# Kernel tuning notes

Hardware: AMD Instinct MI355X
Metric: run time of the kernel (lower is better)

The kernel has to match this reference:

```python
import jax, jax.numpy as jnp
import numpy as np

D = 4096      # feature_dim
L = 24        # num_vision_layers
N = 576       # patches per layer (24x24 grid)
T = 128       # text tokens
RED = D // 4  # DSU reduced dim
TOPK = 128
FINAL_K = 64
THRESH = 2.0
EPS = 1e-6


def _ln(x, eps=1e-5):
    mu = jnp.mean(x, axis=-1, keepdims=True)
    var = jnp.mean((x - mu) ** 2, axis=-1, keepdims=True)
    return (x - mu) / jnp.sqrt(var + eps)


def setup_inputs() -> dict:
    key = jax.random.key(0)
    ks = jax.random.split(key, 8)
    w = lambda k, shape: jax.random.normal(k, shape, jnp.float32) * 0.02
    z = lambda shape: jnp.zeros(shape, jnp.float32)
    return {
        "text_features": jax.random.normal(ks[0], (T, D), jnp.float32),
        "proj": jax.random.normal(ks[1], (L, N, D), jnp.float32),
        "Wq": w(ks[2], (D, D)),
        "Wk": w(ks[3], (D, D)),
        "ln_w": jnp.ones((D,), jnp.float32),
        "ln_b": z((D,)),
        "W1_w": w(ks[4], (RED, 3 * D)), "W1_b": z((RED,)),
        "Wc_w": w(ks[5], (D, RED)), "Wc_b": z((D,)),
        "Wi_w": w(ks[6], (D, RED)), "Wi_b": z((D,)),
        "Wf_w": w(ks[7], (D, RED)), "Wf_b": z((D,)),
        "bc": z((D,)), "bi": z((D,)), "bf": z((D,)),
    }


def _scores_z(text_features, proj, Wq, Wk, ln_w, ln_b,
              W1_w, W1_b, Wc_w, Wc_b, Wi_w, Wi_b, Wf_w, Wf_b, bc, bi, bf):
    # DSU recurrence over layers on (D,) vectors
    text_global = _ln(jnp.mean(text_features, axis=0))  # [D]
    y = jnp.mean(proj, axis=1)                           # [L, D]

    def step(c_prev, y_l):
        combined = jnp.concatenate([jax.nn.sigmoid(c_prev), y_l, text_global])
        s = jax.nn.relu(combined @ W1_w.T + W1_b)
        c_t = jnp.tanh(s @ Wc_w.T + Wc_b + bc)
        i = jax.nn.sigmoid(s @ Wi_w.T + Wi_b + bi)
        f = jax.nn.sigmoid(s @ Wf_w.T + Wf_b + bf)
        c = f * c_prev + i * c_t
        return c, c

    _, contexts = jax.lax.scan(step, jnp.zeros((D,), proj.dtype), y)
    c_final = contexts[-2]
    q = _ln(c_final @ Wq.T) * ln_w + ln_b              # [D]
    k = _ln(jnp.einsum('lnd,ed->lne', proj, Wk)) * ln_w + ln_b  # [L,N,D]
    scores = jnp.einsum('lne,e->ln', k, q)             # [L, N]
    mu = jnp.mean(scores, axis=-1, keepdims=True)
    sd = jnp.std(scores, axis=-1, keepdims=True)       # unbiased=False
    return (scores - mu) / (sd + EPS)


def _select(scores_z_np):
    """Host-side, data-dependent top-k budget allocation (mirrors torch code).
    Returns flat (layer_id, patch_idx) arrays of the final selected evidence."""
    Lc, Nc = scores_z_np.shape
    focus = (-2) % Lc
    conf = scores_z_np.max(axis=-1)
    active = [li for li in range(Lc) if li == focus or conf[li] > THRESH]
    focus_cand = min(TOPK // 2, Nc)
    k_per = [0] * Lc
    k_per[focus] = focus_cand
    rest = max(TOPK - focus_cand, 0)
    other = [li for li in active if li != focus]
    if other and rest > 0:
        cv = conf[other]
        w = np.exp(cv - cv.max()); w = w / w.sum()
        alloc = np.floor(w * rest).astype(np.int64)
        rem = rest - int(alloc.sum())
        for j in np.argsort(-w):
            if rem <= 0:
                break
            alloc[j] += 1; rem -= 1
        for j, li in enumerate(other):
            if alloc[j] > 0:
                k_per[li] = min(int(alloc[j]), Nc)
    li_flat, idx_flat, sc_flat = [], [], []
    for li in range(Lc):
        k_li = min(k_per[li], Nc)
        if k_li <= 0:
            continue
        idx = np.argsort(-scores_z_np[li])[:k_li]   # topk, sorted desc
        li_flat.append(np.full(k_li, li, np.int64))
        idx_flat.append(idx)
        sc_flat.append(scores_z_np[li][idx])
    li_flat = np.concatenate(li_flat)
    idx_flat = np.concatenate(idx_flat)
    sc = np.concatenate(sc_flat)
    M = sc.shape[0]
    final_k = min(FINAL_K, M)
    focus_min = min(FINAL_K // 2, final_k)
    fidx = np.nonzero(li_flat == focus)[0]
    selected = []
    if fidx.size > 0 and focus_min > 0:
        order = np.argsort(-sc[fidx])[:min(focus_min, fidx.size)]
        selected.append(fidx[order])
    remain = final_k - (selected[0].size if selected else 0)
    if remain > 0:
        keep = np.ones(M, bool)
        if selected:
            keep[selected[0]] = False
        cand = np.nonzero(keep)[0]
        order = np.argsort(-sc[cand])[:min(remain, cand.size)]
        selected.append(cand[order])
    sel = np.concatenate(selected) if selected else np.zeros(0, np.int64)
    sel = sel[np.argsort(-sc[sel])]  # final re-sort by score desc
    return li_flat[sel], idx_flat[sel]


def reference(text_features, proj, Wq, Wk, ln_w, ln_b,
              W1_w, W1_b, Wc_w, Wc_b, Wi_w, Wi_b, Wf_w, Wf_b, bc, bi, bf):
    scores_z = _scores_z(text_features, proj, Wq, Wk, ln_w, ln_b,
                         W1_w, W1_b, Wc_w, Wc_b, Wi_w, Wi_b, Wf_w, Wf_b,
                         bc, bi, bf)
    li, idx = _select(np.asarray(scores_z))
    # evidence tokens: gather selected patches across layers -> [final_k, D]
    return proj[jnp.asarray(li), jnp.asarray(idx)]
```

## Files before the change

kernel.cpp:

```cpp
#include <hip/hip_runtime.h>
#include <stdint.h>
#include <math.h>

#define DD 4096
#define LL 24
#define NP 576
#define TT 128
#define RED 1024
#define MTOT (LL * NP)

#define NEG_INF (-3.402823466e+38f)

typedef __bf16 bf16x8 __attribute__((ext_vector_type(8)));
typedef float f32x4 __attribute__((ext_vector_type(4)));

__device__ inline unsigned short bf16_rn(float a) {
  unsigned u = __float_as_uint(a);
  return (unsigned short)((u + 0x7FFFu + ((u >> 16) & 1u)) >> 16);
}
__device__ inline void bsplit(float a, unsigned short& h, unsigned short& l) {
  unsigned short hb = bf16_rn(a);
  float hf = __uint_as_float(((unsigned)hb) << 16);
  h = hb;
  l = bf16_rn(a - hf);
}
__device__ inline float wave_sum(float v) {
  #pragma unroll
  for (int off = 32; off > 0; off >>= 1) v += __shfl_down(v, off);
  return v;
}
__device__ inline float sigm(float x) { return 1.0f / (1.0f + expf(-x)); }

__device__ inline float np_sum(const float* a, int n) {
  if (n < 8) {
    float r = 0.0f;
    for (int i = 0; i < n; ++i) r += a[i];
    return r;
  }
  float r0 = a[0], r1 = a[1], r2 = a[2], r3 = a[3];
  float r4 = a[4], r5 = a[5], r6 = a[6], r7 = a[7];
  int i = 8;
  for (; i + 8 <= n; i += 8) {
    r0 += a[i + 0]; r1 += a[i + 1]; r2 += a[i + 2]; r3 += a[i + 3];
    r4 += a[i + 4]; r5 += a[i + 5]; r6 += a[i + 6]; r7 += a[i + 7];
  }
  float res = ((r0 + r1) + (r2 + r3)) + ((r4 + r5) + (r6 + r7));
  for (; i < n; ++i) res += a[i];
  return res;
}

__global__ __launch_bounds__(256) void k_text_mean(const float4* __restrict__ tf, float4* __restrict__ tmean) {
  int i = blockIdx.x * 256 + threadIdx.x;
  float a = 0, b = 0, c = 0, d = 0;
  for (int t = 0; t < TT; ++t) {
    float4 v = tf[(size_t)t * (DD / 4) + i];
    a += v.x; b += v.y; c += v.z; d += v.w;
  }
  float4 o; o.x = a * (1.0f / TT); o.y = b * (1.0f / TT); o.z = c * (1.0f / TT); o.w = d * (1.0f / TT);
  tmean[i] = o;
}

__global__ __launch_bounds__(256) void k_ln_vec(const float* __restrict__ in, float* __restrict__ out) {
  __shared__ float red[256];
  int tid = threadIdx.x;
  float s = 0;
  for (int i = tid; i < DD; i += 256) s += in[i];
  red[tid] = s; __syncthreads();
  for (int o = 128; o > 0; o >>= 1) { if (tid < o) red[tid] += red[tid + o]; __syncthreads(); }
  float mu = red[0] / (float)DD;
  __syncthreads();
  float v = 0;
  for (int i = tid; i < DD; i += 256) { float d0 = in[i] - mu; v += d0 * d0; }
  red[tid] = v; __syncthreads();
  for (int o = 128; o > 0; o >>= 1) { if (tid < o) red[tid] += red[tid + o]; __syncthreads(); }
  float isd = 1.0f / sqrtf(red[0] / (float)DD + 1e-5f);
  for (int i = tid; i < DD; i += 256) out[i] = (in[i] - mu) * isd;
}

__global__ __launch_bounds__(256) void k_y_mean(const float4* __restrict__ proj, float4* __restrict__ y) {
  int i4 = blockIdx.x * 256 + threadIdx.x;
  int l = i4 >> 10;
  int d4 = i4 & 1023;
  const float4* base = proj + (size_t)l * NP * (DD / 4) + d4;
  float a = 0, b = 0, c = 0, d = 0;
  for (int n = 0; n < NP; ++n) {
    float4 v = base[(size_t)n * (DD / 4)];
    a += v.x; b += v.y; c += v.z; d += v.w;
  }
  float4 o; o.x = a * (1.0f / NP); o.y = b * (1.0f / NP); o.z = c * (1.0f / NP); o.w = d * (1.0f / NP);
  y[i4] = o;
}

__global__ __launch_bounds__(256) void k_base1(const float* __restrict__ W1, const float* __restrict__ W1bias,
                                               const float* __restrict__ y, const float* __restrict__ tg,
                                               float* __restrict__ base1) {
  const int r = blockIdx.x;
  const int tid = threadIdx.x;
  const float* rowB = W1 + (size_t)r * (3 * DD) + DD;
  const float* rowC = W1 + (size_t)r * (3 * DD) + 2 * DD;
  float part[LL];
  #pragma unroll
  for (int l = 0; l < LL; ++l) part[l] = 0.0f;
  float ptg = 0.0f;
  for (int d = tid; d < DD; d += 256) {
    float wb = rowB[d], wc = rowC[d];
    ptg += wc * tg[d];
    #pragma unroll
    for (int l = 0; l < LL; ++l) part[l] += wb * y[l * DD + d];
  }
  __shared__ float red[4 * 25];
  int wv = tid >> 6, lane = tid & 63;
  #pragma unroll
  for (int l = 0; l < LL; ++l) {
    float v = wave_sum(part[l]);
    if (lane == 0) red[wv * 25 + l] = v;
  }
  {
    float v = wave_sum(ptg);
    if (lane == 0) red[wv * 25 + 24] = v;
  }
  __syncthreads();
  if (tid < LL) {
    float v = red[tid] + red[25 + tid] + red[50 + tid] + red[75 + tid];
    float t = red[24] + red[49] + red[74] + red[99];
    base1[tid * RED + r] = v + t + W1bias[r];
  }
}

__global__ __launch_bounds__(256) void k_init(float* __restrict__ c0, float* __restrict__ sg0) {
  int i = blockIdx.x * 256 + threadIdx.x;
  if (i < DD) { c0[i] = 0.0f; sg0[i] = 0.5f; }
}

__global__ __launch_bounds__(256) void k_dsu_A(const float4* __restrict__ W1, const float4* __restrict__ sigc,
                                               const float* __restrict__ base1l, float* __restrict__ s_out) {
  const int r = blockIdx.x;
  const int tid = threadIdx.x;
  const float4* row = W1 + (size_t)r * (3 * DD / 4);
  float acc = 0.0f;
  #pragma unroll
  for (int i = tid; i < DD / 4; i += 256) {
    float4 w = row[i], x = sigc[i];
    acc += w.x * x.x + w.y * x.y + w.z * x.z + w.w * x.w;
  }
  acc = wave_sum(acc);
  __shared__ float red[4];
  if ((tid & 63) == 0) red[tid >> 6] = acc;
  __syncthreads();
  if (tid == 0) {
    float v = red[0] + red[1] + red[2] + red[3] + base1l[r];
    s_out[r] = fmaxf(v, 0.0f);
  }
}

__global__ __launch_bounds__(192) void k_dsu_B(const float4* __restrict__ Wc, const float4* __restrict__ Wi,
                                               const float4* __restrict__ Wf, const float* __restrict__ Wcb,
                                               const float* __restrict__ Wib, const float* __restrict__ Wfb,
                                               const float* __restrict__ bcv, const float* __restrict__ biv,
                                               const float* __restrict__ bfv, const float4* __restrict__ s,
                                               const float* __restrict__ c_in, float* __restrict__ c_out,
                                               float* __restrict__ sigc_out) {
  const int d = blockIdx.x;
  const int wv = threadIdx.x / 64, lane = threadIdx.x & 63;
  const float4* W = (wv == 0) ? Wc : (wv == 1) ? Wi : Wf;
  const float4* row = W + (size_t)d * (RED / 4);
  float acc = 0.0f;
  #pragma unroll
  for (int i = lane; i < RED / 4; i += 64) {
    float4 w = row[i], x = s[i];
    acc += w.x * x.x + w.y * x.y + w.z * x.z + w.w * x.w;
  }
  acc = wave_sum(acc);
  __shared__ float us[3];
  if (lane == 0) us[wv] = acc;
  __syncthreads();
  if (threadIdx.x == 0) {
    float ct = tanhf(us[0] + Wcb[d] + bcv[d]);
    float ig = sigm(us[1] + Wib[d] + biv[d]);
    float fg = sigm(us[2] + Wfb[d] + bfv[d]);
    float c = fg * c_in[d] + ig * ct;
    c_out[d] = c;
    sigc_out[d] = sigm(c);
  }
}

__global__ __launch_bounds__(256) void k_qvec(const float4* __restrict__ Wq, const float4* __restrict__ c,
                                              float* __restrict__ u) {
  const int e = blockIdx.x;
  const int tid = threadIdx.x;
  const float4* row = Wq + (size_t)e * (DD / 4);
  float acc = 0.0f;
  #pragma unroll
  for (int i = tid; i < DD / 4; i += 256) {
    float4 w = row[i], x = c[i];
    acc += w.x * x.x + w.y * x.y + w.z * x.z + w.w * x.w;
  }
  acc = wave_sum(acc);
  __shared__ float red[4];
  if ((tid & 63) == 0) red[tid >> 6] = acc;
  __syncthreads();
  if (tid == 0) u[e] = red[0] + red[1] + red[2] + red[3];
}

__global__ __launch_bounds__(256) void k_qln(const float* __restrict__ u, const float* __restrict__ lnw,
                                             const float* __restrict__ lnb, float* __restrict__ wtil,
                                             float* __restrict__ scal) {
  __shared__ float red[256];
  int tid = threadIdx.x;
  float s = 0;
  for (int i = tid; i < DD; i += 256) s += u[i];
  red[tid] = s; __syncthreads();
  for (int o = 128; o > 0; o >>= 1) { if (tid < o) red[tid] += red[tid + o]; __syncthreads(); }
  float mu = red[0] / (float)DD;
  __syncthreads();
  float v = 0;
  for (int i = tid; i < DD; i += 256) { float d0 = u[i] - mu; v += d0 * d0; }
  red[tid] = v; __syncthreads();
  for (int o = 128; o > 0; o >>= 1) { if (tid < o) red[tid] += red[tid + o]; __syncthreads(); }
  float isd = 1.0f / sqrtf(red[0] / (float)DD + 1e-5f);
  __syncthreads();
  float a = 0, b = 0;
  for (int i = tid; i < DD; i += 256) {
    float q = (u[i] - mu) * isd * lnw[i] + lnb[i];
    float wt = lnw[i] * q;
    wtil[i] = wt;
    a += wt;
    b += lnb[i] * q;
  }
  red[tid] = a; __syncthreads();
  for (int o = 128; o > 0; o >>= 1) { if (tid < o) red[tid] += red[tid + o]; __syncthreads(); }
  float alpha = red[0];
  __syncthreads();
  red[tid] = b; __syncthreads();
  for (int o = 128; o > 0; o >>= 1) { if (tid < o) red[tid] += red[tid + o]; __syncthreads(); }
  if (tid == 0) { scal[0] = alpha; scal[1] = red[0]; }
}

__global__ __launch_bounds__(256) void k_split(const float4* __restrict__ src, ushort4* __restrict__ hi,
                                               ushort4* __restrict__ lo) {
  size_t i = (size_t)blockIdx.x * 256 + threadIdx.x;
  float4 v = src[i];
  ushort4 h, l;
  bsplit(v.x, h.x, l.x);
  bsplit(v.y, h.y, l.y);
  bsplit(v.z, h.z, l.z);
  bsplit(v.w, h.w, l.w);
  hi[i] = h;
  lo[i] = l;
}

#define GLDS16(g, l)                                                                     \
  __builtin_amdgcn_global_load_lds((__attribute__((address_space(1))) void*)(void*)(g),  \
                                   (__attribute__((address_space(3))) void*)(l), 16, 0, 0)

__global__ __launch_bounds__(256) void k_gemm(const unsigned short* __restrict__ Ahi,
                                              const unsigned short* __restrict__ Alo,
                                              const unsigned short* __restrict__ Bhi,
                                              const unsigned short* __restrict__ Blo,
                                              const float* __restrict__ wtilde,
                                              float* __restrict__ partials) {
  __shared__ __align__(16) unsigned short sAh[4096];
  __shared__ __align__(16) unsigned short sAl[4096];
  __shared__ __align__(16) unsigned short sBh[4096];
  __shared__ __align__(16) unsigned short sBl[4096];

  const int tid = threadIdx.x;
  const int w = tid >> 6, lane = tid & 63;
  const int n0 = blockIdx.x * 128, m0 = blockIdx.y * 128;

  const int flat = w * 1024 + lane * 16;
  const int row0 = flat >> 6;
  const int colb = (flat & 63) >> 1;

  const unsigned short* gA0h = Ahi + (size_t)(m0 + row0) * DD + colb;
  const unsigned short* gA1h = gA0h + (size_t)64 * DD;
  const unsigned short* gA0l = Alo + (size_t)(m0 + row0) * DD + colb;
  const unsigned short* gA1l = gA0l + (size_t)64 * DD;
  const unsigned short* gB0h = Bhi + (size_t)(n0 + row0) * DD + colb;
  const unsigned short* gB1h = gB0h + (size_t)64 * DD;
  const unsigned short* gB0l = Blo + (size_t)(n0 + row0) * DD + colb;
  const unsigned short* gB1l = gB0l + (size_t)64 * DD;

  const int r16 = lane & 15, qd = lane >> 4;
  const int wm = (w & 1) << 6, wn = (w >> 1) << 6;

  f32x4 acc[4][4];
  #pragma unroll
  for (int mi = 0; mi < 4; ++mi)
    #pragma unroll
    for (int ni = 0; ni < 4; ++ni) acc[mi][ni] = (f32x4){0.f, 0.f, 0.f, 0.f};

  for (int kk = 0; kk < DD / 32; ++kk) {
    __syncthreads();
    GLDS16(gA0h, sAh + w * 512);
    GLDS16(gA1h, sAh + 2048 + w * 512);
    GLDS16(gA0l, sAl + w * 512);
    GLDS16(gA1l, sAl + 2048 + w * 512);
    GLDS16(gB0h, sBh + w * 512);
    GLDS16(gB1h, sBh + 2048 + w * 512);
    GLDS16(gB0l, sBl + w * 512);
    GLDS16(gB1l, sBl + 2048 + w * 512);
    gA0h += 32; gA1h += 32; gA0l += 32; gA1l += 32;
    gB0h += 32; gB1h += 32; gB0l += 32; gB1l += 32;
    __syncthreads();

    bf16x8 ah[4], al[4], bh[4], bl[4];
    #pragma unroll
    for (int mi = 0; mi < 4; ++mi) {
      int off = (wm + mi * 16 + r16) * 32 + qd * 8;
      ah[mi] = *(const bf16x8*)(sAh + off);
      al[mi] = *(const bf16x8*)(sAl + off);
    }
    #pragma unroll
    for (int ni = 0; ni < 4; ++ni) {
      int off = (wn + ni * 16 + r16) * 32 + qd * 8;
      bh[ni] = *(const bf16x8*)(sBh + off);
      bl[ni] = *(const bf16x8*)(sBl + off);
    }
    #pragma unroll
    for (int mi = 0; mi < 4; ++mi)
      #pragma unroll
      for (int ni = 0; ni < 4; ++ni)
        acc[mi][ni] = __builtin_amdgcn_mfma_f32_16x16x32_bf16(ah[mi], bh[ni], acc[mi][ni], 0, 0, 0);
    #pragma unroll
    for (int mi = 0; mi < 4; ++mi)
      #pragma unroll
      for (int ni = 0; ni < 4; ++ni)
        acc[mi][ni] = __builtin_amdgcn_mfma_f32_16x16x32_bf16(ah[mi], bl[ni], acc[mi][ni], 0, 0, 0);
    #pragma unroll
    for (int mi = 0; mi < 4; ++mi)
      #pragma unroll
      for (int ni = 0; ni < 4; ++ni)
        acc[mi][ni] = __builtin_amdgcn_mfma_f32_16x16x32_bf16(al[mi], bh[ni], acc[mi][ni], 0, 0, 0);
  }

  float wt[4];
  #pragma unroll
  for (int ni = 0; ni < 4; ++ni) wt[ni] = wtilde[n0 + wn + ni * 16 + r16];

  __syncthreads();
  float* epi = (float*)sAh;
  #pragma unroll
  for (int mi = 0; mi < 4; ++mi) {
    #pragma unroll
    for (int j = 0; j < 4; ++j) {
      float sv = 0, sv2 = 0, svw = 0;
      #pragma unroll
      for (int ni = 0; ni < 4; ++ni) {
        float v = acc[mi][ni][j];
        sv += v;
        sv2 += v * v;
        svw += v * wt[ni];
      }
      #pragma unroll
      for (int off = 1; off < 16; off <<= 1) {
        sv += __shfl_xor(sv, off);
        sv2 += __shfl_xor(sv2, off);
        svw += __shfl_xor(svw, off);
      }
      if (r16 == 0) {
        int row = wm + mi * 16 + qd * 4 + j;
        int half = w >> 1;
        epi[(half * 128 + row) * 3 + 0] = sv;
        epi[(half * 128 + row) * 3 + 1] = sv2;
        epi[(half * 128 + row) * 3 + 2] = svw;
      }
    }
  }
  __syncthreads();
  if (tid < 128) {
    size_t base = (size_t)(m0 + tid) * 96 + (size_t)blockIdx.x * 3;
    #pragma unroll
    for (int c = 0; c < 3; ++c) partials[base + c] = epi[tid * 3 + c] + epi[(128 + tid) * 3 + c];
  }
}

__global__ __launch_bounds__(256) void k_scorefin(const float* __restrict__ partials,
                                                  const float* __restrict__ scal,
                                                  float* __restrict__ scores) {
  int m = blockIdx.x * 256 + threadIdx.x;
  const float* p = partials + (size_t)m * 96;
  float s1 = 0, s2 = 0, sw = 0;
  #pragma unroll
  for (int j = 0; j < 32; ++j) {
    s1 += p[j * 3 + 0];
    s2 += p[j * 3 + 1];
    sw += p[j * 3 + 2];
  }
  float mu = s1 * (1.0f / DD);
  float var = s2 * (1.0f / DD) - mu * mu;
  float isd = 1.0f / sqrtf(var + 1e-5f);
  scores[m] = isd * (sw - mu * scal[0]) + scal[1];
}

__global__ __launch_bounds__(256) void k_zscore(const float* __restrict__ scores, float* __restrict__ z,
                                                float* __restrict__ conf) {
  const int l = blockIdx.x;
  const int tid = threadIdx.x;
  const float* s = scores + l * NP;
  __shared__ float red[256];
  float a = 0;
  for (int i = tid; i < NP; i += 256) a += s[i];
  red[tid] = a; __syncthreads();
  for (int o = 128; o > 0; o >>= 1) { if (tid < o) red[tid] += red[tid + o]; __syncthreads(); }
  float mu = red[0] / (float)NP;
  __syncthreads();
  float v = 0;
  for (int i = tid; i < NP; i += 256) { float d0 = s[i] - mu; v += d0 * d0; }
  red[tid] = v; __syncthreads();
  for (int o = 128; o > 0; o >>= 1) { if (tid < o) red[tid] += red[tid + o]; __syncthreads(); }
  float sd = sqrtf(red[0] / (float)NP);
  float inv = 1.0f / (sd + 1e-6f);
  __syncthreads();
  float mx = NEG_INF;
  for (int i = tid; i < NP; i += 256) {
    float zz = (s[i] - mu) * inv;
    z[l * NP + i] = zz;
    mx = fmaxf(mx, zz);
  }
  red[tid] = mx; __syncthreads();
  for (int o = 128; o > 0; o >>= 1) { if (tid < o) red[tid] = fmaxf(red[tid], red[tid + o]); __syncthreads(); }
  if (tid == 0) conf[l] = red[0];
}

__global__ __launch_bounds__(64) void k_select(const float* __restrict__ z, const float* __restrict__ conf,
                                               int* __restrict__ sel_li, int* __restrict__ sel_idx) {
  const int lane = threadIdx.x;
  __shared__ int kper[24];
  __shared__ int offs[25];
  __shared__ float zb[576];
  __shared__ float csc[160];
  __shared__ int cli[160];
  __shared__ int cidx[160];
  __shared__ int taken[160];
  __shared__ int selpos[64];

  if (lane == 0) {
    const int focus = 22;
    float cf[24];
    for (int l = 0; l < 24; ++l) cf[l] = conf[l];
    int other[24]; int no = 0;
    for (int l = 0; l < 24; ++l)
      if (l != focus && cf[l] > 2.0f) other[no++] = l;
    int kp[24];
    for (int l = 0; l < 24; ++l) kp[l] = 0;
    kp[focus] = 64;
    const int rest = 64;
    if (no > 0) {
      float wv[24];
      float cmax = cf[other[0]];
      for (int j = 1; j < no; ++j) cmax = fmaxf(cmax, cf[other[j]]);
      for (int j = 0; j < no; ++j) wv[j] = (float)exp((double)(cf[other[j]] - cmax));
      float wsum = np_sum(wv, no);
      for (int j = 0; j < no; ++j) wv[j] = wv[j] / wsum;
      int alloc[24]; int asum = 0;
      for (int j = 0; j < no; ++j) { alloc[j] = (int)floorf(wv[j] * 64.0f); asum += alloc[j]; }
      int rem = rest - asum;
      int used[24];
      for (int j = 0; j < no; ++j) used[j] = 0;
      for (int t = 0; t < no && rem > 0; ++t) {
        int bj = -1; float bw = -1e38f;
        for (int j = 0; j < no; ++j)
          if (!used[j] && wv[j] > bw) { bw = wv[j]; bj = j; }
        used[bj] = 1; alloc[bj] += 1; rem -= 1;
      }
      for (int j = 0; j < no; ++j)
        if (alloc[j] > 0) kp[other[j]] = (alloc[j] < NP) ? alloc[j] : NP;
    }
    int o = 0;
    for (int l = 0; l < 24; ++l) { kper[l] = kp[l]; offs[l] = o; o += kp[l]; }
    offs[24] = o;
  }
  __syncthreads();

  for (int l = 0; l < 24; ++l) {
    const int kl = kper[l];
    if (kl == 0) continue;
    for (int i = lane; i < NP; i += 64) zb[i] = z[l * NP + i];
    __syncthreads();
    const int base = offs[l];
    for (int t = 0; t < kl; ++t) {
      float bv = NEG_INF; int bi_ = 0x7fffffff;
      for (int i = lane; i < NP; i += 64) {
        float v = zb[i];
        if (v > bv) { bv = v; bi_ = i; }
      }
      #pragma unroll
      for (int off = 32; off > 0; off >>= 1) {
        float ov = __shfl_down(bv, off);
        int oi = __shfl_down(bi_, off);
        if (ov > bv || (ov == bv && oi < bi_)) { bv = ov; bi_ = oi; }
      }
      bv = __shfl(bv, 0);
      bi_ = __shfl(bi_, 0);
      if (lane == 0) {
        csc[base + t] = bv; cli[base + t] = l; cidx[base + t] = bi_;
        zb[bi_] = NEG_INF;
      }
      __syncthreads();
    }
    __syncthreads();
  }

  const int M = offs[24];
  const int foff = offs[22];
  for (int i = lane; i < M; i += 64) taken[i] = 0;
  __syncthreads();
  if (lane < 32) { selpos[lane] = foff + lane; taken[foff + lane] = 1; }
  __syncthreads();
  for (int t = 0; t < 32; ++t) {
    float bv = NEG_INF; int bp = 0x7fffffff;
    for (int i = lane; i < M; i += 64) {
      if (!taken[i]) {
        float v = csc[i];
        if (v > bv || (v == bv && i < bp)) { bv = v; bp = i; }
      }
    }
    #pragma unroll
    for (int off = 32; off > 0; off >>= 1) {
      float ov = __shfl_down(bv, off);
      int op = __shfl_down(bp, off);
      if (ov > bv || (ov == bv && op < bp)) { bv = ov; bp = op; }
    }
    bp = __shfl(bp, 0);
    if (lane == 0) { selpos[32 + t] = bp; taken[bp] = 1; }
    __syncthreads();
  }
  if (lane == 0) {
    int a = 0, b = 32;
    for (int k = 0; k < 64; ++k) {
      bool takeA;
      if (a >= 32) takeA = false;
      else if (b >= 64) takeA = true;
      else takeA = (csc[selpos[a]] >= csc[selpos[b]]);
      int p = takeA ? selpos[a++] : selpos[b++];
      sel_li[k] = cli[p];
      sel_idx[k] = cidx[p];
    }
  }
}

__global__ __launch_bounds__(256) void k_gather(const float4* __restrict__ proj, const int* __restrict__ sel_li,
                                                const int* __restrict__ sel_idx, float4* __restrict__ out) {
  int r = blockIdx.x;
  int li = sel_li[r], idx = sel_idx[r];
  const float4* src = proj + (size_t)(li * NP + idx) * (DD / 4);
  float4* dst = out + (size_t)r * (DD / 4);
  for (int i = threadIdx.x; i < DD / 4; i += 256) dst[i] = src[i];
}

constexpr size_t OFF_AHI = 0;
constexpr size_t OFF_ALO = OFF_AHI + 113246208ull;
constexpr size_t OFF_BHI = OFF_ALO + 113246208ull;
constexpr size_t OFF_BLO = OFF_BHI + 33554432ull;
constexpr size_t OFF_PART = OFF_BLO + 33554432ull;
constexpr size_t OFF_SCORE = OFF_PART + 5308416ull;
constexpr size_t OFF_Z = OFF_SCORE + 55296ull;
constexpr size_t OFF_TMEAN = OFF_Z + 55296ull;
constexpr size_t OFF_TG = OFF_TMEAN + 16384ull;
constexpr size_t OFF_Y = OFF_TG + 16384ull;
constexpr size_t OFF_BASE1 = OFF_Y + 393216ull;
constexpr size_t OFF_CA = OFF_BASE1 + 98304ull;
constexpr size_t OFF_CB = OFF_CA + 16384ull;
constexpr size_t OFF_SGA = OFF_CB + 16384ull;
constexpr size_t OFF_SGB = OFF_SGA + 16384ull;
constexpr size_t OFF_S = OFF_SGB + 16384ull;
constexpr size_t OFF_U = OFF_S + 4096ull;
constexpr size_t OFF_WT = OFF_U + 16384ull;
constexpr size_t OFF_SCAL = OFF_WT + 16384ull;
constexpr size_t OFF_CONF = OFF_SCAL + 256ull;
constexpr size_t OFF_SELLI = OFF_CONF + 256ull;
constexpr size_t OFF_SELIX = OFF_SELLI + 256ull;

extern "C" void kernel_launch(void* const* d_in, const int* in_sizes, int n_in,
                              void* d_out, int out_size, void* d_ws, size_t ws_size,
                              hipStream_t stream) {
  (void)in_sizes; (void)n_in; (void)out_size; (void)ws_size;
  const float* tf = (const float*)d_in[0];
  const float* proj = (const float*)d_in[1];
  const float* Wq = (const float*)d_in[2];
  const float* Wk = (const float*)d_in[3];
  const float* ln_w = (const float*)d_in[4];
  const float* ln_b = (const float*)d_in[5];
  const float* W1w = (const float*)d_in[6];
  const float* W1b = (const float*)d_in[7];
  const float* Wcw = (const float*)d_in[8];
  const float* Wcb = (const float*)d_in[9];
  const float* Wiw = (const float*)d_in[10];
  const float* Wib = (const float*)d_in[11];
  const float* Wfw = (const float*)d_in[12];
  const float* Wfb = (const float*)d_in[13];
  const float* bc = (const float*)d_in[14];
  const float* bi = (const float*)d_in[15];
  const float* bf = (const float*)d_in[16];

  char* ws = (char*)d_ws;
  unsigned short* Ahi = (unsigned short*)(ws + OFF_AHI);
  unsigned short* Alo = (unsigned short*)(ws + OFF_ALO);
  unsigned short* Bhi = (unsigned short*)(ws + OFF_BHI);
  unsigned short* Blo = (unsigned short*)(ws + OFF_BLO);
  float* partials = (float*)(ws + OFF_PART);
  float* scores = (float*)(ws + OFF_SCORE);
  float* zbuf = (float*)(ws + OFF_Z);
  float* tmean = (float*)(ws + OFF_TMEAN);
  float* tg = (float*)(ws + OFF_TG);
  float* ybuf = (float*)(ws + OFF_Y);
  float* base1 = (float*)(ws + OFF_BASE1);
  float* cA = (float*)(ws + OFF_CA);
  float* cB = (float*)(ws + OFF_CB);
  float* sgA = (float*)(ws + OFF_SGA);
  float* sgB = (float*)(ws + OFF_SGB);
  float* svec = (float*)(ws + OFF_S);
  float* uvec = (float*)(ws + OFF_U);
  float* wtil = (float*)(ws + OFF_WT);
  float* scal = (float*)(ws + OFF_SCAL);
  float* conf = (float*)(ws + OFF_CONF);
  int* sel_li = (int*)(ws + OFF_SELLI);
  int* sel_idx = (int*)(ws + OFF_SELIX);

  k_text_mean<<<4, 256, 0, stream>>>((const float4*)tf, (float4*)tmean);
  k_ln_vec<<<1, 256, 0, stream>>>(tmean, tg);
  k_y_mean<<<96, 256, 0, stream>>>((const float4*)proj, (float4*)ybuf);
  k_base1<<<1024, 256, 0, stream>>>(W1w, W1b, ybuf, tg, base1);
  k_init<<<16, 256, 0, stream>>>(cA, sgA);

  float* cbuf[2] = {cA, cB};
  float* sgbuf[2] = {sgA, sgB};
  for (int l = 0; l < 23; ++l) {
    int pi = l & 1;
    k_dsu_A<<<1024, 256, 0, stream>>>((const float4*)W1w, (const float4*)sgbuf[pi],
                                      base1 + (size_t)l * RED, svec);
    k_dsu_B<<<4096, 192, 0, stream>>>((const float4*)Wcw, (const float4*)Wiw, (const float4*)Wfw,
                                      Wcb, Wib, Wfb, bc, bi, bf,
                                      (const float4*)svec, cbuf[pi], cbuf[1 - pi], sgbuf[1 - pi]);
  }
  k_qvec<<<4096, 256, 0, stream>>>((const float4*)Wq, (const float4*)cbuf[1], uvec);
  k_qln<<<1, 256, 0, stream>>>(uvec, ln_w, ln_b, wtil, scal);

  k_split<<<55296, 256, 0, stream>>>((const float4*)proj, (ushort4*)Ahi, (ushort4*)Alo);
  k_split<<<16384, 256, 0, stream>>>((const float4*)Wk, (ushort4*)Bhi, (ushort4*)Blo);

  k_gemm<<<dim3(32, 108), 256, 0, stream>>>(Ahi, Alo, Bhi, Blo, wtil, partials);

  k_scorefin<<<54, 256, 0, stream>>>(partials, scal, scores);
  k_zscore<<<24, 256, 0, stream>>>(scores, zbuf, conf);
  k_select<<<1, 64, 0, stream>>>(zbuf, conf, sel_li, sel_idx);
  k_gather<<<64, 256, 0, stream>>>((const float4*)proj, sel_li, sel_idx, (float4*)d_out);
}
```

Baseline: 2.443 ms.

## Fuse DSU recurrence into persistent kernel with grid barriers, overlap bf16 split

Replaces the 46 per-layer DSU launches plus the qvec and qln kernels with one persistent kernel of 256 blocks that synchronises through atomic grid barriers. A second group of 256 blocks in the same launch runs the bf16 hi/lo split of proj and Wk while the serial recurrence proceeds. This is meant to remove launch overhead and tail idle time from the latency-bound recurrence and hide the split's memory traffic behind it. The risks are deadlock if all 512 blocks are not co-resident, spin-barrier latency, and the split blocks competing with the recurrence for bandwidth.

```diff
diff --git a/kernel.cpp b/kernel.cpp
--- a/kernel.cpp
+++ b/kernel.cpp
@@ -11,6 +11,9 @@
 
 #define NEG_INF (-3.402823466e+38f)
 
+#define NDSU 256
+#define NSPL 256
+
 typedef __bf16 bf16x8 __attribute__((ext_vector_type(8)));
 typedef float f32x4 __attribute__((ext_vector_type(4)));
 
@@ -30,6 +33,18 @@
   return v;
 }
 __device__ inline float sigm(float x) { return 1.0f / (1.0f + expf(-x)); }
+
+__device__ inline void gbar(unsigned* ctr, unsigned nblk) {
+  __syncthreads();
+  if (threadIdx.x == 0) {
+    __threadfence();
+    __hip_atomic_fetch_add(ctr, 1u, __ATOMIC_RELEASE, __HIP_MEMORY_SCOPE_AGENT);
+    while (__hip_atomic_load(ctr, __ATOMIC_ACQUIRE, __HIP_MEMORY_SCOPE_AGENT) < nblk)
+      __builtin_amdgcn_s_sleep(8);
+    __threadfence();
+  }
+  __syncthreads();
+}
 
 __device__ inline float np_sum(const float* a, int n) {
   if (n < 8) {
@@ -127,126 +142,155 @@
   }
 }
 
-__global__ __launch_bounds__(256) void k_init(float* __restrict__ c0, float* __restrict__ sg0) {
+__global__ __launch_bounds__(256) void k_init(float* __restrict__ c0, float* __restrict__ sg0,
+                                              unsigned* __restrict__ bar) {
   int i = blockIdx.x * 256 + threadIdx.x;
   if (i < DD) { c0[i] = 0.0f; sg0[i] = 0.5f; }
-}
-
-__global__ __launch_bounds__(256) void k_dsu_A(const float4* __restrict__ W1, const float4* __restrict__ sigc,
-                                               const float* __restrict__ base1l, float* __restrict__ s_out) {
-  const int r = blockIdx.x;
+  if (blockIdx.x == 0 && threadIdx.x < 64) bar[threadIdx.x] = 0u;
+}
+
+__global__ __launch_bounds__(256, 4) void k_fused(
+    const float4* __restrict__ W1,
+    const float* __restrict__ base1,
+    const float4* __restrict__ Wc, const float4* __restrict__ Wi, const float4* __restrict__ Wf,
+    const float* __restrict__ Wcb, const float* __restrict__ Wib, const float* __restrict__ Wfb,
+    const float* __restrict__ bcv, const float* __restrict__ biv, const float* __restrict__ bfv,
+    const float4* __restrict__ Wq,
+    const float* __restrict__ lnw, const float* __restrict__ lnb,
+    float* __restrict__ cA, float* __restrict__ cB,
+    float* __restrict__ sgA, float* __restrict__ sgB,
+    float* __restrict__ svec, float* __restrict__ uvec,
+    float* __restrict__ wtil, float* __restrict__ scal,
+    unsigned* __restrict__ bar,
+    const float4* __restrict__ proj4, const float4* __restrict__ Wk4,
+    ushort4* __restrict__ Ahi, ushort4* __restrict__ Alo,
+    ushort4* __restrict__ Bhi, ushort4* __restrict__ Blo) {
+  const int bid = blockIdx.x;
   const int tid = threadIdx.x;
-  const float4* row = W1 + (size_t)r * (3 * DD / 4);
-  float acc = 0.0f;
-  #pragma unroll
-  for (int i = tid; i < DD / 4; i += 256) {
-    float4 w = row[i], x = sigc[i];
-    acc += w.x * x.x + w.y * x.y + w.z * x.z + w.w * x.w;
-  }
-  acc = wave_sum(acc);
-  __shared__ float red[4];
-  if ((tid & 63) == 0) red[tid >> 6] = acc;
-  __syncthreads();
-  if (tid == 0) {
-    float v = red[0] + red[1] + red[2] + red[3] + base1l[r];
-    s_out[r] = fmaxf(v, 0.0f);
-  }
-}
-
-__global__ __launch_bounds__(192) void k_dsu_B(const float4* __restrict__ Wc, const float4* __restrict__ Wi,
-                                               const float4* __restrict__ Wf, const float* __restrict__ Wcb,
-                                               const float* __restrict__ Wib, const float* __restrict__ Wfb,
-                                               const float* __restrict__ bcv, const float* __restrict__ biv,
-                                               const float* __restrict__ bfv, const float4* __restrict__ s,
-                                               const float* __restrict__ c_in, float* __restrict__ c_out,
-                                               float* __restrict__ sigc_out) {
-  const int d = blockIdx.x;
-  const int wv = threadIdx.x / 64, lane = threadIdx.x & 63;
-  const float4* W = (wv == 0) ? Wc : (wv == 1) ? Wi : Wf;
-  const float4* row = W + (size_t)d * (RED / 4);
-  float acc = 0.0f;
-  #pragma unroll
-  for (int i = lane; i < RED / 4; i += 64) {
-    float4 w = row[i], x = s[i];
-    acc += w.x * x.x + w.y * x.y + w.z * x.z + w.w * x.w;
-  }
-  acc = wave_sum(acc);
-  __shared__ float us[3];
-  if (lane == 0) us[wv] = acc;
-  __syncthreads();
-  if (threadIdx.x == 0) {
-    float ct = tanhf(us[0] + Wcb[d] + bcv[d]);
-    float ig = sigm(us[1] + Wib[d] + biv[d]);
-    float fg = sigm(us[2] + Wfb[d] + bfv[d]);
-    float c = fg * c_in[d] + ig * ct;
-    c_out[d] = c;
-    sigc_out[d] = sigm(c);
-  }
-}
-
-__global__ __launch_bounds__(256) void k_qvec(const float4* __restrict__ Wq, const float4* __restrict__ c,
-                                              float* __restrict__ u) {
-  const int e = blockIdx.x;
-  const int tid = threadIdx.x;
-  const float4* row = Wq + (size_t)e * (DD / 4);
-  float acc = 0.0f;
-  #pragma unroll
-  for (int i = tid; i < DD / 4; i += 256) {
-    float4 w = row[i], x = c[i];
-    acc += w.x * x.x + w.y * x.y + w.z * x.z + w.w * x.w;
-  }
-  acc = wave_sum(acc);
-  __shared__ float red[4];
-  if ((tid & 63) == 0) red[tid >> 6] = acc;
-  __syncthreads();
-  if (tid == 0) u[e] = red[0] + red[1] + red[2] + red[3];
-}
-
-__global__ __launch_bounds__(256) void k_qln(const float* __restrict__ u, const float* __restrict__ lnw,
-                                             const float* __restrict__ lnb, float* __restrict__ wtil,
-                                             float* __restrict__ scal) {
-  __shared__ float red[256];
-  int tid = threadIdx.x;
-  float s = 0;
-  for (int i = tid; i < DD; i += 256) s += u[i];
-  red[tid] = s; __syncthreads();
-  for (int o = 128; o > 0; o >>= 1) { if (tid < o) red[tid] += red[tid + o]; __syncthreads(); }
-  float mu = red[0] / (float)DD;
-  __syncthreads();
-  float v = 0;
-  for (int i = tid; i < DD; i += 256) { float d0 = u[i] - mu; v += d0 * d0; }
-  red[tid] = v; __syncthreads();
-  for (int o = 128; o > 0; o >>= 1) { if (tid < o) red[tid] += red[tid + o]; __syncthreads(); }
-  float isd = 1.0f / sqrtf(red[0] / (float)DD + 1e-5f);
-  __syncthreads();
-  float a = 0, b = 0;
-  for (int i = tid; i < DD; i += 256) {
-    float q = (u[i] - mu) * isd * lnw[i] + lnb[i];
-    float wt = lnw[i] * q;
-    wtil[i] = wt;
-    a += wt;
-    b += lnb[i] * q;
-  }
-  red[tid] = a; __syncthreads();
-  for (int o = 128; o > 0; o >>= 1) { if (tid < o) red[tid] += red[tid + o]; __syncthreads(); }
-  float alpha = red[0];
-  __syncthreads();
-  red[tid] = b; __syncthreads();
-  for (int o = 128; o > 0; o >>= 1) { if (tid < o) red[tid] += red[tid + o]; __syncthreads(); }
-  if (tid == 0) { scal[0] = alpha; scal[1] = red[0]; }
-}
-
-__global__ __launch_bounds__(256) void k_split(const float4* __restrict__ src, ushort4* __restrict__ hi,
-                                               ushort4* __restrict__ lo) {
-  size_t i = (size_t)blockIdx.x * 256 + threadIdx.x;
-  float4 v = src[i];
-  ushort4 h, l;
-  bsplit(v.x, h.x, l.x);
-  bsplit(v.y, h.y, l.y);
-  bsplit(v.z, h.z, l.z);
-  bsplit(v.w, h.w, l.w);
-  hi[i] = h;
-  lo[i] = l;
+
+  if (bid >= NDSU) {
+    const size_t stride = (size_t)NSPL * 256;
+    size_t i0 = (size_t)(bid - NDSU) * 256 + tid;
+    for (size_t i = i0; i < 14155776ull; i += stride) {
+      float4 v = proj4[i];
+      ushort4 h, l;
+      bsplit(v.x, h.x, l.x); bsplit(v.y, h.y, l.y);
+      bsplit(v.z, h.z, l.z); bsplit(v.w, h.w, l.w);
+      Ahi[i] = h; Alo[i] = l;
+    }
+    for (size_t i = i0; i < 4194304ull; i += stride) {
+      float4 v = Wk4[i];
+      ushort4 h, l;
+      bsplit(v.x, h.x, l.x); bsplit(v.y, h.y, l.y);
+      bsplit(v.z, h.z, l.z); bsplit(v.w, h.w, l.w);
+      Bhi[i] = h; Blo[i] = l;
+    }
+    return;
+  }
+
+  const int wv = tid >> 6, lane = tid & 63;
+
+  for (int l = 0; l < 23; ++l) {
+    const float* sg_in = (l & 1) ? sgB : sgA;
+    const float* c_in  = (l & 1) ? cB : cA;
+    float* c_out  = (l & 1) ? cA : cB;
+    float* sg_out = (l & 1) ? sgA : sgB;
+
+    {
+      const int r = bid * 4 + wv;
+      const float4* row = W1 + (size_t)r * (3 * DD / 4);
+      const float4* x4 = (const float4*)sg_in;
+      float acc = 0.0f;
+      #pragma unroll
+      for (int i = 0; i < 16; ++i) {
+        float4 w = row[lane + i * 64];
+        float4 x = x4[lane + i * 64];
+        acc += w.x * x.x + w.y * x.y + w.z * x.z + w.w * x.w;
+      }
+      acc = wave_sum(acc);
+      if (lane == 0) svec[r] = fmaxf(acc + base1[l * RED + r], 0.0f);
+    }
+    gbar(&bar[2 * l], NDSU);
+
+    {
+      const float4* s4 = (const float4*)svec;
+      #pragma unroll
+      for (int j = 0; j < 4; ++j) {
+        const int d = bid * 16 + wv * 4 + j;
+        float aC = 0, aI = 0, aF = 0;
+        #pragma unroll
+        for (int i = 0; i < 4; ++i) {
+          float4 x = s4[lane + i * 64];
+          float4 wc_ = Wc[(size_t)d * (RED / 4) + lane + i * 64];
+          float4 wi_ = Wi[(size_t)d * (RED / 4) + lane + i * 64];
+          float4 wf_ = Wf[(size_t)d * (RED / 4) + lane + i * 64];
+          aC += wc_.x * x.x + wc_.y * x.y + wc_.z * x.z + wc_.w * x.w;
+          aI += wi_.x * x.x + wi_.y * x.y + wi_.z * x.z + wi_.w * x.w;
+          aF += wf_.x * x.x + wf_.y * x.y + wf_.z * x.z + wf_.w * x.w;
+        }
+        aC = wave_sum(aC); aI = wave_sum(aI); aF = wave_sum(aF);
+        if (lane == 0) {
+          float ct = tanhf(aC + Wcb[d] + bcv[d]);
+          float ig = sigm(aI + Wib[d] + biv[d]);
+          float fg = sigm(aF + Wfb[d] + bfv[d]);
+          float c = fg * c_in[d] + ig * ct;
+          c_out[d] = c;
+          sg_out[d] = sigm(c);
+        }
+      }
+    }
+    gbar(&bar[2 * l + 1], NDSU);
+  }
+
+  {
+    const float4* cf = (const float4*)cB;
+    #pragma unroll
+    for (int j = 0; j < 4; ++j) {
+      const int e = bid * 16 + wv * 4 + j;
+      const float4* row = Wq + (size_t)e * (DD / 4);
+      float acc = 0.0f;
+      #pragma unroll
+      for (int i = 0; i < 16; ++i) {
+        float4 w = row[lane + i * 64];
+        float4 x = cf[lane + i * 64];
+        acc += w.x * x.x + w.y * x.y + w.z * x.z + w.w * x.w;
+      }
+      acc = wave_sum(acc);
+      if (lane == 0) uvec[e] = acc;
+    }
+  }
+  gbar(&bar[46], NDSU);
+
+  if (bid == 0) {
+    __shared__ float red[256];
+    float s = 0;
+    for (int i = tid; i < DD; i += 256) s += uvec[i];
+    red[tid] = s; __syncthreads();
+    for (int o = 128; o > 0; o >>= 1) { if (tid < o) red[tid] += red[tid + o]; __syncthreads(); }
+    float mu = red[0] / (float)DD;
+    __syncthreads();
+    float v = 0;
+    for (int i = tid; i < DD; i += 256) { float d0 = uvec[i] - mu; v += d0 * d0; }
+    red[tid] = v; __syncthreads();
+    for (int o = 128; o > 0; o >>= 1) { if (tid < o) red[tid] += red[tid + o]; __syncthreads(); }
+    float isd = 1.0f / sqrtf(red[0] / (float)DD + 1e-5f);
+    __syncthreads();
+    float a = 0, b = 0;
+    for (int i = tid; i < DD; i += 256) {
+      float q = (uvec[i] - mu) * isd * lnw[i] + lnb[i];
+      float wt = lnw[i] * q;
+      wtil[i] = wt;
+      a += wt;
+      b += lnb[i] * q;
+    }
+    red[tid] = a; __syncthreads();
+    for (int o = 128; o > 0; o >>= 1) { if (tid < o) red[tid] += red[tid + o]; __syncthreads(); }
+    float alpha = red[0];
+    __syncthreads();
+    red[tid] = b; __syncthreads();
+    for (int o = 128; o > 0; o >>= 1) { if (tid < o) red[tid] += red[tid + o]; __syncthreads(); }
+    if (tid == 0) { scal[0] = alpha; scal[1] = red[0]; }
+  }
 }
 
 #define GLDS16(g, l)                                                                     \
@@ -571,6 +615,7 @@
 constexpr size_t OFF_CONF = OFF_SCAL + 256ull;
 constexpr size_t OFF_SELLI = OFF_CONF + 256ull;
 constexpr size_t OFF_SELIX = OFF_SELLI + 256ull;
+constexpr size_t OFF_BAR = OFF_SELIX + 256ull;
 
 extern "C" void kernel_launch(void* const* d_in, const int* in_sizes, int n_in,
                               void* d_out, int out_size, void* d_ws, size_t ws_size,
@@ -617,28 +662,22 @@
   float* conf = (float*)(ws + OFF_CONF);
   int* sel_li = (int*)(ws + OFF_SELLI);
   int* sel_idx = (int*)(ws + OFF_SELIX);
+  unsigned* bar = (unsigned*)(ws + OFF_BAR);
 
   k_text_mean<<<4, 256, 0, stream>>>((const float4*)tf, (float4*)tmean);
   k_ln_vec<<<1, 256, 0, stream>>>(tmean, tg);
   k_y_mean<<<96, 256, 0, stream>>>((const float4*)proj, (float4*)ybuf);
   k_base1<<<1024, 256, 0, stream>>>(W1w, W1b, ybuf, tg, base1);
-  k_init<<<16, 256, 0, stream>>>(cA, sgA);
-
-  float* cbuf[2] = {cA, cB};
-  float* sgbuf[2] = {sgA, sgB};
-  for (int l = 0; l < 23; ++l) {
-    int pi = l & 1;
-    k_dsu_A<<<1024, 256, 0, stream>>>((const float4*)W1w, (const float4*)sgbuf[pi],
-                                      base1 + (size_t)l * RED, svec);
-    k_dsu_B<<<4096, 192, 0, stream>>>((const float4*)Wcw, (const float4*)Wiw, (const float4*)Wfw,
-                                      Wcb, Wib, Wfb, bc, bi, bf,
-                                      (const float4*)svec, cbuf[pi], cbuf[1 - pi], sgbuf[1 - pi]);
-  }
-  k_qvec<<<4096, 256, 0, stream>>>((const float4*)Wq, (const float4*)cbuf[1], uvec);
-  k_qln<<<1, 256, 0, stream>>>(uvec, ln_w, ln_b, wtil, scal);
-
-  k_split<<<55296, 256, 0, stream>>>((const float4*)proj, (ushort4*)Ahi, (ushort4*)Alo);
-  k_split<<<16384, 256, 0, stream>>>((const float4*)Wk, (ushort4*)Bhi, (ushort4*)Blo);
+  k_init<<<16, 256, 0, stream>>>(cA, sgA, bar);
+
+  k_fused<<<NDSU + NSPL, 256, 0, stream>>>(
+      (const float4*)W1w, base1,
+      (const float4*)Wcw, (const float4*)Wiw, (const float4*)Wfw,
+      Wcb, Wib, Wfb, bc, bi, bf,
+      (const float4*)Wq, ln_w, ln_b,
+      cA, cB, sgA, sgB, svec, uvec, wtil, scal, bar,
+      (const float4*)proj, (const float4*)Wk,
+      (ushort4*)Ahi, (ushort4*)Alo, (ushort4*)Bhi, (ushort4*)Blo);
 
   k_gemm<<<dim3(32, 108), 256, 0, stream>>>(Ahi, Alo, Bhi, Blo, wtil, partials);
 
```

Result: slower. 3.999 ms (+63.7%).
